# Kernel tuning notes

Measured on AMD Instinct MI355X. Metric: run time of the kernel, lower is better.

## Reference

```python
import jax, jax.numpy as jnp
import numpy as np

N, E = 50000, 300000
IN, FC, AC, H, C1, C2, OUT = 1024, 128, 20, 4, 10, 5, 3
FCN = FC + AC + H * C2  # 168


def bn_eval(x, g, b):
    # BatchNorm1d in eval mode with running_mean=0, running_var=1
    return x * (g / jnp.sqrt(1.0 + 1e-5)) + b


def add_self_loops(edge_index, edge_attr, n):
    # PyG add_self_loops with fill_value='mean': self-loop attr = mean of incoming edge attrs
    src, dst = edge_index[0], edge_index[1]
    ones = jnp.ones(src.shape[0], jnp.float32)
    deg = jax.ops.segment_sum(ones, dst, num_segments=n)
    mean_attr = jax.ops.segment_sum(edge_attr, dst, num_segments=n) / jnp.maximum(deg, 1.0)[:, None]
    loop = jnp.arange(n, dtype=src.dtype)
    return (jnp.concatenate([src, loop]), jnp.concatenate([dst, loop]),
            jnp.concatenate([edge_attr, mean_attr], 0))


def gatv2(x, src, dst, eattr, Wl, bl, Wr, br, We, att, b, n):
    # GATv2Conv (concat=True, negative_slope=0.2, edge_dim=1)
    h, c = att.shape
    xl = (x @ Wl + bl).reshape(n, h, c)
    xr = (x @ Wr + br).reshape(n, h, c)
    em = (eattr @ We).reshape(-1, h, c)
    m = jax.nn.leaky_relu(xl[src] + xr[dst] + em, 0.2)   # [E', H, C]
    logit = jnp.einsum('ehc,hc->eh', m, att)              # [E', H]
    mx = jax.ops.segment_max(logit, dst, num_segments=n)
    ex = jnp.exp(logit - mx[dst])
    den = jax.ops.segment_sum(ex, dst, num_segments=n)
    alpha = ex / (den[dst] + 1e-16)                       # segment softmax over dst
    out = jax.ops.segment_sum(xl[src] * alpha[..., None], dst, num_segments=n)
    return out.reshape(n, h * c) + b


def setup_inputs() -> dict:
    key = jax.random.key(0)
    ks = jax.random.split(key, 24)
    rn = lambda k, s: jax.random.normal(k, s, jnp.float32) * 0.05
    return {
        'features': jax.random.normal(ks[0], (N, IN), jnp.float32),
        'edges': jax.random.randint(ks[1], (2, E), 0, N),
        'edges2': jax.random.randint(ks[2], (2, E), 0, N),
        'edge_features': jax.random.normal(ks[3], (E, 1), jnp.float32),
        'additional_features': jax.random.normal(ks[4], (N, AC), jnp.float32),
        'sage_Wl': rn(ks[5], (IN, FC)), 'sage_bl': jnp.zeros((FC,), jnp.float32),
        'sage_Wr': rn(ks[6], (IN, FC)),
        'g1_Wl': rn(ks[7], (AC, H * C1)), 'g1_bl': jnp.zeros((H * C1,), jnp.float32),
        'g1_Wr': rn(ks[8], (AC, H * C1)), 'g1_br': jnp.zeros((H * C1,), jnp.float32),
        'g1_We': rn(ks[9], (1, H * C1)), 'g1_att': rn(ks[10], (H, C1)),
        'g1_b': jnp.zeros((H * C1,), jnp.float32),
        'g2_Wl': rn(ks[11], (H * C1, H * C2)), 'g2_bl': jnp.zeros((H * C2,), jnp.float32),
        'g2_Wr': rn(ks[12], (H * C1, H * C2)), 'g2_br': jnp.zeros((H * C2,), jnp.float32),
        'g2_We': rn(ks[13], (1, H * C2)), 'g2_att': rn(ks[14], (H, C2)),
        'g2_b': jnp.zeros((H * C2,), jnp.float32),
        'fc1_W': rn(ks[15], (FCN, FCN)), 'fc1_b': jnp.zeros((FCN,), jnp.float32),
        'fc2_W': rn(ks[16], (FCN, OUT)), 'fc2_b': jnp.zeros((OUT,), jnp.float32),
        'bnx_g': jnp.ones((FC,), jnp.float32), 'bnx_b': jnp.zeros((FC,), jnp.float32),
        'bny_g': jnp.ones((H * C2,), jnp.float32), 'bny_b': jnp.zeros((H * C2,), jnp.float32),
        'bnf_g': jnp.ones((FCN,), jnp.float32), 'bnf_b': jnp.zeros((FCN,), jnp.float32),
    }


def reference(features, edges, edges2, edge_features, additional_features,
              sage_Wl, sage_bl, sage_Wr,
              g1_Wl, g1_bl, g1_Wr, g1_br, g1_We, g1_att, g1_b,
              g2_Wl, g2_bl, g2_Wr, g2_br, g2_We, g2_att, g2_b,
              fc1_W, fc1_b, fc2_W, fc2_b,
              bnx_g, bnx_b, bny_g, bny_b, bnf_g, bnf_b):
    n = features.shape[0]
    # --- SAGEConv (mean aggr): out = lin_l(mean_j x_j) + lin_r(x_i) ---
    src, dst = edges[0], edges[1]
    deg = jax.ops.segment_sum(jnp.ones(src.shape[0], jnp.float32), dst, num_segments=n)
    aggr = jax.ops.segment_sum(features[src], dst, num_segments=n) / jnp.maximum(deg, 1.0)[:, None]
    x = aggr @ sage_Wl + sage_bl + features @ sage_Wr
    x = bn_eval(x, bnx_g, bnx_b)
    # --- GATv2 stack (self loops with mean edge-attr fill) ---
    s2, d2, ea = add_self_loops(edges2, edge_features, n)
    y = gatv2(additional_features, s2, d2, ea, g1_Wl, g1_bl, g1_Wr, g1_br, g1_We, g1_att, g1_b, n)
    y = jax.nn.leaky_relu(y, 0.01)  # activation (dropout off in eval)
    y = gatv2(y, s2, d2, ea, g2_Wl, g2_bl, g2_Wr, g2_br, g2_We, g2_att, g2_b, n)
    y = bn_eval(y, bny_g, bny_b)
    # --- MLP head ---
    z = jax.nn.leaky_relu(jnp.concatenate([x, y], axis=1), 0.01)
    z = jnp.concatenate([z, additional_features], axis=1) @ fc1_W + fc1_b
    z = jax.nn.relu(bn_eval(z, bnf_g, bnf_b))
    return z @ fc2_W + fc2_b
```

## Files before the change

### kernel.cpp

```cpp
#include <hip/hip_runtime.h>
#include <hip/hip_bf16.h>
#include <cfloat>

__device__ __forceinline__ float lrelu(float x, float a) { return x > 0.0f ? x : a * x; }

__device__ __forceinline__ unsigned short f2bf(float f) {
    unsigned u = __float_as_uint(f);
    unsigned r = (u + 0x7FFFu + ((u >> 16) & 1u)) >> 16;
    return (unsigned short)r;
}
__device__ __forceinline__ float bf2f(unsigned short u) {
    return __uint_as_float((unsigned)u << 16);
}

typedef __attribute__((ext_vector_type(8))) short short8;
typedef __attribute__((ext_vector_type(4))) float f32x4;

#define BN_RSQ 0.99999500003749968750f
#define SCAN_B 256

__global__ void zero_ws(uint4* __restrict__ p, int n16)
{
    int t = blockIdx.x * blockDim.x + threadIdx.x;
    if (t < n16) p[t] = make_uint4(0u, 0u, 0u, 0u);
// ... 45 lines not shown
        int j = idx & 7, lane = (idx >> 3) & 63, q = idx >> 9;
        int fn = q % 3, t = q / 3;
        int c = fn * 16 + (lane & 15);
        int k = t * 32 + (lane >> 4) * 8 + j;
        float v = 0.0f;
        if (k < 40 && c < 40) v = (c < 20) ? g2Wl[(size_t)k * 20 + c] : g2Wr[(size_t)k * 20 + (c - 20)];
        Bg2[idx] = f2bf(v);
        return;
    }
    idx -= 3072;
    if (idx < E) {
        atomicAdd(&cnt1[e1d[idx]], 1);
        int d2 = e2d[idx];
        atomicAdd(&cnt2[d2], 1);
        atomicAdd(&easum[d2], ef[idx]);
    }
}

__global__ __launch_bounds__(256) void gemm_sage_mfma(
    const float* __restrict__ A, const unsigned short* __restrict__ Btp,
    unsigned short* __restrict__ P, int M)
{
    __shared__ unsigned short As2[2][64][72];
    const int tid = threadIdx.x;
    const int wid = tid >> 6, lane = tid & 63;
    const int m0 = blockIdx.x * 64;
    const int l16 = lane & 15, g = lane >> 4;
    const int colbase = wid * 64 + l16;
    const short8* Bv = reinterpret_cast<const short8*>(Btp);
    const int srow = tid >> 4, scol = (tid & 15) * 4;

    f32x4 acc[4][4] = {};
    float4 rcur[4], rnext[4];

#pragma unroll
    for (int p = 0; p < 4; ++p) {
        int ar = m0 + p * 16 + srow;
        rcur[p] = make_float4(0.f, 0.f, 0.f, 0.f);
        if (ar < M) rcur[p] = *reinterpret_cast<const float4*>(&A[(size_t)ar * 1024 + scol]);
    }
#pragma unroll
    for (int p = 0; p < 4; ++p) {
        ushort4 u;
        u.x = f2bf(rcur[p].x); u.y = f2bf(rcur[p].y); u.z = f2bf(rcur[p].z); u.w = f2bf(rcur[p].w);
        *reinterpret_cast<ushort4*>(&As2[0][p * 16 + srow][scol]) = u;
    }
#pragma unroll
    for (int p = 0; p < 4; ++p) {
        int ar = m0 + p * 16 + srow;
        rcur[p] = make_float4(0.f, 0.f, 0.f, 0.f);
        if (ar < M) rcur[p] = *reinterpret_cast<const float4*>(&A[(size_t)ar * 1024 + 64 + scol]);
    }
    __syncthreads();

    for (int c = 0; c < 16; ++c) {
        const int buf = c & 1;
        if (c < 14) {
            const int k0 = (c + 2) * 64;
#pragma unroll
            for (int p = 0; p < 4; ++p) {
                int ar = m0 + p * 16 + srow;
                rnext[p] = make_float4(0.f, 0.f, 0.f, 0.f);
                if (ar < M) rnext[p] = *reinterpret_cast<const float4*>(&A[(size_t)ar * 1024 + k0 + scol]);
            }
        }
#pragma unroll
        for (int t = 0; t < 2; ++t) {
            const int ks = c * 2 + t;
            short8 afr[4], bfr[4];
#pragma unroll
            for (int fm = 0; fm < 4; ++fm)
                afr[fm] = *reinterpret_cast<const short8*>(&As2[buf][fm * 16 + l16][t * 32 + g * 8]);
#pragma unroll
            for (int fn = 0; fn < 4; ++fn)
                bfr[fn] = Bv[((ks * 4 + wid) * 4 + fn) * 64 + lane];
#pragma unroll
            for (int fm = 0; fm < 4; ++fm)
#pragma unroll
                for (int fn = 0; fn < 4; ++fn)
                    acc[fm][fn] = __builtin_amdgcn_mfma_f32_16x16x32_bf16(
                        afr[fm], bfr[fn], acc[fm][fn], 0, 0, 0);
        }
        if (c < 15) {
#pragma unroll
            for (int p = 0; p < 4; ++p) {
                ushort4 u;
                u.x = f2bf(rcur[p].x); u.y = f2bf(rcur[p].y);
                u.z = f2bf(rcur[p].z); u.w = f2bf(rcur[p].w);
                *reinterpret_cast<ushort4*>(&As2[buf ^ 1][p * 16 + srow][scol]) = u;
            }
        }
        __syncthreads();
#pragma unroll
        for (int p = 0; p < 4; ++p) rcur[p] = rnext[p];
    }

#pragma unroll
    for (int fm = 0; fm < 4; ++fm) {
#pragma unroll
        for (int r = 0; r < 4; ++r) {
            int row = m0 + fm * 16 + g * 4 + r;
            if (row < M) {
#pragma unroll
                for (int fn = 0; fn < 4; ++fn)
                    P[(size_t)row * 256 + colbase + fn * 16] = f2bf(acc[fm][fn][r]);
            }
        }
    }
}

template <int IND, int KS, int NF, int MODE>
__global__ __launch_bounds__(64) void gat_lin_mfma(
    const float* __restrict__ X, const unsigned short* __restrict__ Bp,
    const float* __restrict__ bl, const float* __restrict__ br,
    float* __restrict__ xl, float* __restrict__ xr, int M)
{
    constexpr int W = KS * 32;
    constexpr int WP = W + 8;
    __shared__ unsigned short xs[64][WP];
    const int lane = threadIdx.x;
    const int m0 = blockIdx.x * 64;
    const int l16 = lane & 15, g = lane >> 4;
    const short8* Bv = reinterpret_cast<const short8*>(Bp);

    constexpr int NV = 64 * IND / 4 / 64;
#pragma unroll
    for (int i = 0; i < NV; ++i) {
        int q = i * 64 + lane;
        int f = q * 4;
        int row = f / IND, col = f % IND;
        int ar = m0 + row;
        float4 v = make_float4(0.f, 0.f, 0.f, 0.f);
        if (ar < M) v = *reinterpret_cast<const float4*>(&X[(size_t)ar * IND + col]);
        ushort4 u;
        u.x = f2bf(v.x); u.y = f2bf(v.y); u.z = f2bf(v.z); u.w = f2bf(v.w);
        *reinterpret_cast<ushort4*>(&xs[row][col]) = u;
    }
    ushort4 zz; zz.x = 0; zz.y = 0; zz.z = 0; zz.w = 0;
#pragma unroll
    for (int c = IND; c < W; c += 4)
        *reinterpret_cast<ushort4*>(&xs[lane][c]) = zz;

    f32x4 acc[4][NF] = {};
#pragma unroll
    for (int t = 0; t < KS; ++t) {
        short8 afr[4], bfr[NF];
#pragma unroll
        for (int fm = 0; fm < 4; ++fm)
            afr[fm] = *reinterpret_cast<const short8*>(&xs[fm * 16 + l16][t * 32 + g * 8]);
#pragma unroll
        for (int fn = 0; fn < NF; ++fn)
            bfr[fn] = Bv[(t * NF + fn) * 64 + lane];
#pragma unroll
        for (int fm = 0; fm < 4; ++fm)
#pragma unroll
            for (int fn = 0; fn < NF; ++fn)
                acc[fm][fn] = __builtin_amdgcn_mfma_f32_16x16x32_bf16(
                    afr[fm], bfr[fn], acc[fm][fn], 0, 0, 0);
    }

#pragma unroll
    for (int fm = 0; fm < 4; ++fm) {
#pragma unroll
        for (int r = 0; r < 4; ++r) {
            int row = m0 + fm * 16 + g * 4 + r;
            if (row < M) {
#pragma unroll
                for (int fn = 0; fn < NF; ++fn) {
                    int col = fn * 16 + l16;
                    float v = acc[fm][fn][r];
                    if (MODE == 1) {
                        if (col < 40) {
                            int h = col / 10, c = col % 10;
                            xl[((size_t)row * 4 + h) * 12 + c] = v + bl[col];
                        } else if (col < 80) {
                            int cc = col - 40, h = cc / 10, c = cc % 10;
                            xr[((size_t)row * 4 + h) * 12 + c] = v + br[cc];
                        }
                    } else {
                        if (col < 20) {
                            int h = col / 5, c = col % 5;
                            xl[((size_t)row * 4 + h) * 8 + c] = v + bl[col];
                        } else if (col < 40) {
                            int cc = col - 20, h = cc / 5, c = cc % 5;
                            xr[((size_t)row * 4 + h) * 8 + c] = v + br[cc];
                        }
                    }
                }
            }
        }
    }
}

__global__ __launch_bounds__(256) void mlp_mfma(
    const unsigned short* __restrict__ z, const float* __restrict__ addf,
    const unsigned short* __restrict__ Bt1p,
    const float* __restrict__ fc1b, const float* __restrict__ bnfg, const float* __restrict__ bnfb,
    const float* __restrict__ fc2W, const float* __restrict__ fc2b,
    float* __restrict__ out, int M)
{
    __shared__ __align__(16) char smem[64 * 169 * 4];
    unsigned short (*zs)[200] = reinterpret_cast<unsigned short(*)[200]>(smem);
    float (*ts)[169] = reinterpret_cast<float(*)[169]>(smem);
    const int tid = threadIdx.x;
    const int wid = tid >> 6, lane = tid & 63;
    const int m0 = blockIdx.x * 64;
    const int l16 = lane & 15, g = lane >> 4;
    const short8* Bv = reinterpret_cast<const short8*>(Bt1p);

#pragma unroll
    for (int p = 0; p < 13; ++p) {
        int idx = p * 256 + tid;
        if (idx < 3200) {
            int row = idx / 50, c4 = (idx % 50) * 4;
            int ar = m0 + row;
            ushort4 u; u.x = 0; u.y = 0; u.z = 0; u.w = 0;
            if (ar < M) {
                if (c4 < 148) {
                    u = *reinterpret_cast<const ushort4*>(&z[(size_t)ar * 168 + c4]);
                } else if (c4 < 168) {
                    float4 v = *reinterpret_cast<const float4*>(&addf[(size_t)ar * 20 + (c4 - 148)]);
                    u.x = f2bf(v.x); u.y = f2bf(v.y); u.z = f2bf(v.z); u.w = f2bf(v.w);
                }
            }
            *reinterpret_cast<ushort4*>(&zs[row][c4]) = u;
        }
    }
    __syncthreads();

    f32x4 acc[4][4] = {};
    if (wid < 3) {
#pragma unroll
        for (int t = 0; t < 6; ++t) {
            short8 afr[4], bfr[4];
#pragma unroll
            for (int fm = 0; fm < 4; ++fm)
                afr[fm] = *reinterpret_cast<const short8*>(&zs[fm * 16 + l16][t * 32 + g * 8]);
#pragma unroll
            for (int fn = 0; fn < 4; ++fn)
                bfr[fn] = Bv[((t * 3 + wid) * 4 + fn) * 64 + lane];
#pragma unroll
            for (int fm = 0; fm < 4; ++fm)
#pragma unroll
                for (int fn = 0; fn < 4; ++fn)
                    acc[fm][fn] = __builtin_amdgcn_mfma_f32_16x16x32_bf16(
                        afr[fm], bfr[fn], acc[fm][fn], 0, 0, 0);
        }
    }
    __syncthreads();
    if (wid < 3) {
        const int colbase = wid * 64 + l16;
#pragma unroll
        for (int fm = 0; fm < 4; ++fm) {
#pragma unroll
            for (int r = 0; r < 4; ++r) {
                int rr = fm * 16 + g * 4 + r;
#pragma unroll
                for (int fn = 0; fn < 4; ++fn) {
                    int col = colbase + fn * 16;
                    if (col < 168) {
                        float v = acc[fm][fn][r] + fc1b[col];
                        v = v * (bnfg[col] * BN_RSQ) + bnfb[col];
                        ts[rr][col] = fmaxf(v, 0.0f);
                    }
                }
            }
        }
    }
    __syncthreads();
    if (tid < 192) {
        int r = tid & 63, c = tid >> 6;
        float acc2 = fc2b[c];
#pragma unroll 4
        for (int k = 0; k < 168; ++k) acc2 += ts[r][k] * fc2W[k * 3 + c];
        int row = m0 + r;
        if (row < M) out[(size_t)row * 3 + c] = acc2;
    }
}

__global__ void scan1(const int* __restrict__ cnt1, const int* __restrict__ cnt2,
                      int* __restrict__ off1, int* __restrict__ off2,
                      int* __restrict__ bsum1, int* __restrict__ bsum2, int M)
{
    __shared__ int sh[SCAN_B];
    int y = blockIdx.y;
    const int* cnt = y ? cnt2 : cnt1;
    int* excl = y ? off2 : off1;
    int* bsum = y ? bsum2 : bsum1;
    int i = blockIdx.x * SCAN_B + threadIdx.x;
    int v = (i < M) ? cnt[i] + y : 0;
    sh[threadIdx.x] = v;
// ... 30 lines not shown
                      const float* __restrict__ easum, float* __restrict__ ealoop, int M)
{
    int y = blockIdx.y;
    int* off = y ? off2 : off1;
    const int* bsum = y ? bsum2 : bsum1;
    const int* cnt = y ? cnt2 : cnt1;
    int i = blockIdx.x * SCAN_B + threadIdx.x;
    if (i < M) {
        int v = off[i] + bsum[blockIdx.x];
        off[i] = v;
        if (i == M - 1) off[M] = v + cnt[i] + y;
        if (y) ealoop[i] = easum[i] / fmaxf((float)cnt2[i], 1.0f);
    }
}

__global__ void fill_both(const int* __restrict__ e1s, const int* __restrict__ e1d,
                          const int* __restrict__ e2s, const int* __restrict__ e2d,
                          const float* __restrict__ ef, const float* __restrict__ ealoop,
                          const int* __restrict__ off1, const int* __restrict__ off2,
                          int* __restrict__ cnt1, int* __restrict__ cnt2,
                          int* __restrict__ srcs1, int2* __restrict__ se2, int E, int Eext)
{
    int t = blockIdx.x * blockDim.x + threadIdx.x;
    if (t < E) {
        int d = e1d[t];
        int pos = atomicSub(&cnt1[d], 1) - 1;
        srcs1[off1[d] + pos] = e1s[t];
    }
    int t2 = t - E;
    if (t2 >= 0 && t2 < Eext) {
        if (t2 < E) {
            int d = e2d[t2];
            int pos = atomicSub(&cnt2[d], 1) - 1;
            se2[off2[d] + pos] = make_int2(e2s[t2], __float_as_int(ef[t2]));
        } else {
            int nn = t2 - E;
            se2[off2[nn + 1] - 1] = make_int2(nn, __float_as_int(ealoop[nn]));
        }
    }
}

__global__ void sage_gather(const int* __restrict__ srcs1, const int* __restrict__ off1,
                            const unsigned short* __restrict__ P, const float* __restrict__ bl,
                            const float* __restrict__ bng, const float* __restrict__ bnb,
                            unsigned short* __restrict__ z, int N)
{
    int t = blockIdx.x * blockDim.x + threadIdx.x;
    if (t >= N * 16) return;
    int n = t >> 4, g = t & 15;
    int beg = off1[n], end = off1[n + 1];
    float a[8] = {};
    for (int j = beg; j < end; ++j) {
        int s = srcs1[j];
        short8 v = *reinterpret_cast<const short8*>(&P[(size_t)s * 256 + g * 8]);
#pragma unroll
        for (int k = 0; k < 8; ++k) a[k] += bf2f((unsigned short)v[k]);
    }
    float inv = 1.0f / fmaxf((float)(end - beg), 1.0f);
    short8 pr = *reinterpret_cast<const short8*>(&P[(size_t)n * 256 + 128 + g * 8]);
    short8 zo;
#pragma unroll
    for (int k = 0; k < 8; ++k) {
        int cc = g * 8 + k;
        float x = a[k] * inv + bl[cc] + bf2f((unsigned short)pr[k]);
        x = x * (bng[cc] * BN_RSQ) + bnb[cc];
        zo[k] = (short)f2bf(lrelu(x, 0.01f));
    }
    *reinterpret_cast<short8*>(&z[(size_t)n * 168 + g * 8]) = zo;
}

template <int H, int C, int PAD, int MODE>
__global__ void gat_node(const int2* __restrict__ se2, const int* __restrict__ off2,
                         const float* __restrict__ xl, const float* __restrict__ xr,
                         const float* __restrict__ We, const float* __restrict__ att,
                         const float* __restrict__ b,
                         const float* __restrict__ bng, const float* __restrict__ bnb,
                         void* __restrict__ outv, int N)
{
    int t = blockIdx.x * blockDim.x + threadIdx.x;
    if (t >= N * H) return;
    int n = t / H, h = t % H;

    float xrc[PAD], atth[PAD], weh[PAD];
    const float4* xrp = reinterpret_cast<const float4*>(&xr[((size_t)n * H + h) * PAD]);
#pragma unroll
    for (int q = 0; q < PAD / 4; ++q) {
        float4 v = xrp[q];
        xrc[q * 4 + 0] = v.x; xrc[q * 4 + 1] = v.y; xrc[q * 4 + 2] = v.z; xrc[q * 4 + 3] = v.w;
    }
#pragma unroll
    for (int c = 0; c < PAD; ++c) {
        atth[c] = (c < C) ? att[h * C + c] : 0.0f;
        weh[c]  = (c < C) ? We[h * C + c]  : 0.0f;
    }

    const int beg = off2[n], end = off2[n + 1];

    float mx = -FLT_MAX, den = 0.0f;
    float accv[PAD] = {};
    for (int j = beg; j < end; ++j) {
        int2 se = se2[j];
        int s = se.x;
        float ea = __int_as_float(se.y);
        const float4* xlp = reinterpret_cast<const float4*>(&xl[((size_t)s * H + h) * PAD]);
        float xv[PAD];
#pragma unroll
        for (int q = 0; q < PAD / 4; ++q) {
            float4 v = xlp[q];
            xv[q * 4 + 0] = v.x; xv[q * 4 + 1] = v.y; xv[q * 4 + 2] = v.z; xv[q * 4 + 3] = v.w;
        }
        float lg = 0.0f;
#pragma unroll
        for (int c = 0; c < PAD; ++c) {
            float m = xv[c] + xrc[c] + ea * weh[c];
            lg += lrelu(m, 0.2f) * atth[c];
        }
        if (lg > mx) {
            float sc = __expf(mx - lg);
            den *= sc;
#pragma unroll
            for (int c = 0; c < PAD; ++c) accv[c] *= sc;
            mx = lg;
        }
        float ex = __expf(lg - mx);
        den += ex;
#pragma unroll
        for (int c = 0; c < PAD; ++c) accv[c] += ex * xv[c];
    }
    float inv = 1.0f / (den + 1e-16f);

#pragma unroll
    for (int c = 0; c < C; ++c) {
        int jch = h * C + c;
        float v = accv[c] * inv + b[jch];
        if (MODE == 1) {
            ((float*)outv)[(size_t)n * (H * C) + jch] = lrelu(v, 0.01f);
        } else {
            v = v * (bng[jch] * BN_RSQ) + bnb[jch];
            ((unsigned short*)outv)[(size_t)n * 168 + 128 + jch] = f2bf(lrelu(v, 0.01f));
        }
    }
}

extern "C" void kernel_launch(void* const* d_in, const int* in_sizes, int n_in,
                              void* d_out, int out_size, void* d_ws, size_t ws_size,
                              hipStream_t stream)
{
    const float* features = (const float*)d_in[0];
    const int*   e1       = (const int*)d_in[1];
    const int*   e2       = (const int*)d_in[2];
    const float* ef       = (const float*)d_in[3];
    const float* addf     = (const float*)d_in[4];
    const float* sage_Wl  = (const float*)d_in[5];
    const float* sage_bl  = (const float*)d_in[6];
    const float* sage_Wr  = (const float*)d_in[7];
// ... 23 lines not shown
    const float* bnf_b = (const float*)d_in[31];

    const int N = in_sizes[0] / 1024;
    const int E = in_sizes[3];
    const int Eext = E + N;
    const int* e1s = e1, *e1d = e1 + E;
    const int* e2s = e2, *e2d = e2 + E;
    const int nb = (N + SCAN_B - 1) / SCAN_B;

    char* wb = (char*)d_ws;
    size_t off = 0;
    auto takeB = [&](size_t bytes) { char* p = wb + off; off = (off + bytes + 255) & ~(size_t)255; return p; };
    unsigned short* P = (unsigned short*)takeB((size_t)N * 256 * 2);
    unsigned short* z = (unsigned short*)takeB((size_t)N * 168 * 2);
    float* ealoop = (float*)takeB((size_t)N * 4);
    float* xl1   = (float*)takeB((size_t)N * 48 * 4);
    float* xr1   = (float*)takeB((size_t)N * 48 * 4);
    float* y1    = (float*)takeB((size_t)N * 40 * 4);
    float* xl2   = (float*)takeB((size_t)N * 32 * 4);
    float* xr2   = (float*)takeB((size_t)N * 32 * 4);
    unsigned short* Btp  = (unsigned short*)takeB((size_t)256 * 1024 * 2);
    unsigned short* Bt1p = (unsigned short*)takeB((size_t)36864 * 2);
    unsigned short* Bg1  = (unsigned short*)takeB((size_t)2560 * 2);
    unsigned short* Bg2  = (unsigned short*)takeB((size_t)3072 * 2);
    char* zero_beg = wb + off;
    int* cnt1    = (int*)takeB((size_t)N * 4);
    int* cnt2    = (int*)takeB((size_t)N * 4);
    float* easum = (float*)takeB((size_t)N * 4);
    size_t zero_len = (size_t)((wb + off) - zero_beg);
    int* off1  = (int*)takeB((size_t)(N + 1) * 4);
    int* off2  = (int*)takeB((size_t)(N + 1) * 4);
    int* bsum1 = (int*)takeB(SCAN_B * 4);
    int* bsum2 = (int*)takeB(SCAN_B * 4);
    int* srcs1 = (int*)takeB((size_t)E * 4);
    int2* se2  = (int2*)takeB((size_t)Eext * 8);
// ... 1 lines not shown
    const int B = 256;
    const int n16 = (int)(zero_len / 16);
    zero_ws<<<(n16 + B - 1) / B, B, 0, stream>>>((uint4*)zero_beg, n16);

    const int prep_total = 262144 + 36864 + 2560 + 3072 + E;
    prep_all<<<(prep_total + B - 1) / B, B, 0, stream>>>(
        sage_Wl, sage_Wr, Btp, fc1_W, Bt1p,
        g1_Wl, g1_Wr, Bg1, g2_Wl, g2_Wr, Bg2,
        e1d, e2d, ef, cnt1, cnt2, easum, E);

    scan1<<<dim3(nb, 2), SCAN_B, 0, stream>>>(cnt1, cnt2, off1, off2, bsum1, bsum2, N);
    scan2<<<dim3(1, 2), SCAN_B, 0, stream>>>(bsum1, bsum2, nb);
    scan3<<<dim3(nb, 2), SCAN_B, 0, stream>>>(off1, off2, bsum1, bsum2, cnt1, cnt2,
                                              easum, ealoop, N);

    fill_both<<<(E + Eext + B - 1) / B, B, 0, stream>>>(e1s, e1d, e2s, e2d, ef, ealoop,
                                                        off1, off2, cnt1, cnt2,
                                                        srcs1, se2, E, Eext);

    const int mtiles = (N + 63) / 64;
    gemm_sage_mfma<<<mtiles, 256, 0, stream>>>(features, Btp, P, N);
    sage_gather<<<(N * 16 + B - 1) / B, B, 0, stream>>>(srcs1, off1, P, sage_bl, bnx_g, bnx_b, z, N);

    gat_lin_mfma<20, 1, 5, 1><<<mtiles, 64, 0, stream>>>(addf, Bg1, g1_bl, g1_br, xl1, xr1, N);
    gat_node<4, 10, 12, 1><<<(N * 4 + B - 1) / B, B, 0, stream>>>(
        se2, off2, xl1, xr1, g1_We, g1_att, g1_b, nullptr, nullptr, (void*)y1, N);

    gat_lin_mfma<40, 2, 3, 2><<<mtiles, 64, 0, stream>>>(y1, Bg2, g2_bl, g2_br, xl2, xr2, N);
    gat_node<4, 5, 8, 2><<<(N * 4 + B - 1) / B, B, 0, stream>>>(
        se2, off2, xl2, xr2, g2_We, g2_att, g2_b, bny_g, bny_b, (void*)z, N);

    mlp_mfma<<<mtiles, 256, 0, stream>>>(z, addf, Bt1p, fc1_b, bnf_g, bnf_b, fc2_W, fc2_b,
                                         (float*)d_out, N);
}
```

Before: 296.8 us.

## Merge independent kernels into block-partitioned launches and store GAT projections as bf16

Independent stages (the SAGE GEMM, the CSR fill and the first GAT linear) are merged into one launch that routes each block by its index. The SAGE gather and the first GAT node aggregation share a second launch. This lets independent work overlap and cuts launch gaps. The GAT xl/xr intermediates are now stored in bf16 instead of fp32, which halves gather traffic at some cost in precision.

```diff
diff --git a/kernel.cpp b/kernel.cpp
--- a/kernel.cpp
+++ b/kernel.cpp
@@ -83,267 +83,6 @@
         int d2 = e2d[idx];
         atomicAdd(&cnt2[d2], 1);
         atomicAdd(&easum[d2], ef[idx]);
-    }
-}
-
-__global__ __launch_bounds__(256) void gemm_sage_mfma(
-    const float* __restrict__ A, const unsigned short* __restrict__ Btp,
-    unsigned short* __restrict__ P, int M)
-{
-    __shared__ unsigned short As2[2][64][72];
-    const int tid = threadIdx.x;
-    const int wid = tid >> 6, lane = tid & 63;
-    const int m0 = blockIdx.x * 64;
-    const int l16 = lane & 15, g = lane >> 4;
-    const int colbase = wid * 64 + l16;
-    const short8* Bv = reinterpret_cast<const short8*>(Btp);
-    const int srow = tid >> 4, scol = (tid & 15) * 4;
-
-    f32x4 acc[4][4] = {};
-    float4 rcur[4], rnext[4];
-
-#pragma unroll
-    for (int p = 0; p < 4; ++p) {
-        int ar = m0 + p * 16 + srow;
-        rcur[p] = make_float4(0.f, 0.f, 0.f, 0.f);
-        if (ar < M) rcur[p] = *reinterpret_cast<const float4*>(&A[(size_t)ar * 1024 + scol]);
-    }
-#pragma unroll
-    for (int p = 0; p < 4; ++p) {
-        ushort4 u;
-        u.x = f2bf(rcur[p].x); u.y = f2bf(rcur[p].y); u.z = f2bf(rcur[p].z); u.w = f2bf(rcur[p].w);
-        *reinterpret_cast<ushort4*>(&As2[0][p * 16 + srow][scol]) = u;
-    }
-#pragma unroll
-    for (int p = 0; p < 4; ++p) {
-        int ar = m0 + p * 16 + srow;
-        rcur[p] = make_float4(0.f, 0.f, 0.f, 0.f);
-        if (ar < M) rcur[p] = *reinterpret_cast<const float4*>(&A[(size_t)ar * 1024 + 64 + scol]);
-    }
-    __syncthreads();
-
-    for (int c = 0; c < 16; ++c) {
-        const int buf = c & 1;
-        if (c < 14) {
-            const int k0 = (c + 2) * 64;
-#pragma unroll
-            for (int p = 0; p < 4; ++p) {
-                int ar = m0 + p * 16 + srow;
-                rnext[p] = make_float4(0.f, 0.f, 0.f, 0.f);
-                if (ar < M) rnext[p] = *reinterpret_cast<const float4*>(&A[(size_t)ar * 1024 + k0 + scol]);
-            }
-        }
-#pragma unroll
-        for (int t = 0; t < 2; ++t) {
-            const int ks = c * 2 + t;
-            short8 afr[4], bfr[4];
-#pragma unroll
-            for (int fm = 0; fm < 4; ++fm)
-                afr[fm] = *reinterpret_cast<const short8*>(&As2[buf][fm * 16 + l16][t * 32 + g * 8]);
-#pragma unroll
-            for (int fn = 0; fn < 4; ++fn)
-                bfr[fn] = Bv[((ks * 4 + wid) * 4 + fn) * 64 + lane];
-#pragma unroll
-            for (int fm = 0; fm < 4; ++fm)
-#pragma unroll
-                for (int fn = 0; fn < 4; ++fn)
-                    acc[fm][fn] = __builtin_amdgcn_mfma_f32_16x16x32_bf16(
-                        afr[fm], bfr[fn], acc[fm][fn], 0, 0, 0);
-        }
-        if (c < 15) {
-#pragma unroll
-            for (int p = 0; p < 4; ++p) {
-                ushort4 u;
-                u.x = f2bf(rcur[p].x); u.y = f2bf(rcur[p].y);
-                u.z = f2bf(rcur[p].z); u.w = f2bf(rcur[p].w);
-                *reinterpret_cast<ushort4*>(&As2[buf ^ 1][p * 16 + srow][scol]) = u;
-            }
-        }
-        __syncthreads();
-#pragma unroll
-        for (int p = 0; p < 4; ++p) rcur[p] = rnext[p];
-    }
-
-#pragma unroll
-    for (int fm = 0; fm < 4; ++fm) {
-#pragma unroll
-        for (int r = 0; r < 4; ++r) {
-            int row = m0 + fm * 16 + g * 4 + r;
-            if (row < M) {
-#pragma unroll
-                for (int fn = 0; fn < 4; ++fn)
-                    P[(size_t)row * 256 + colbase + fn * 16] = f2bf(acc[fm][fn][r]);
-            }
-        }
-    }
-}
-
-template <int IND, int KS, int NF, int MODE>
-__global__ __launch_bounds__(64) void gat_lin_mfma(
-    const float* __restrict__ X, const unsigned short* __restrict__ Bp,
-    const float* __restrict__ bl, const float* __restrict__ br,
-    float* __restrict__ xl, float* __restrict__ xr, int M)
-{
-    constexpr int W = KS * 32;
-    constexpr int WP = W + 8;
-    __shared__ unsigned short xs[64][WP];
-    const int lane = threadIdx.x;
-    const int m0 = blockIdx.x * 64;
-    const int l16 = lane & 15, g = lane >> 4;
-    const short8* Bv = reinterpret_cast<const short8*>(Bp);
-
-    constexpr int NV = 64 * IND / 4 / 64;
-#pragma unroll
-    for (int i = 0; i < NV; ++i) {
-        int q = i * 64 + lane;
-        int f = q * 4;
-        int row = f / IND, col = f % IND;
-        int ar = m0 + row;
-        float4 v = make_float4(0.f, 0.f, 0.f, 0.f);
-        if (ar < M) v = *reinterpret_cast<const float4*>(&X[(size_t)ar * IND + col]);
-        ushort4 u;
-        u.x = f2bf(v.x); u.y = f2bf(v.y); u.z = f2bf(v.z); u.w = f2bf(v.w);
-        *reinterpret_cast<ushort4*>(&xs[row][col]) = u;
-    }
-    ushort4 zz; zz.x = 0; zz.y = 0; zz.z = 0; zz.w = 0;
-#pragma unroll
-    for (int c = IND; c < W; c += 4)
-        *reinterpret_cast<ushort4*>(&xs[lane][c]) = zz;
-
-    f32x4 acc[4][NF] = {};
-#pragma unroll
-    for (int t = 0; t < KS; ++t) {
-        short8 afr[4], bfr[NF];
-#pragma unroll
-        for (int fm = 0; fm < 4; ++fm)
-            afr[fm] = *reinterpret_cast<const short8*>(&xs[fm * 16 + l16][t * 32 + g * 8]);
-#pragma unroll
-        for (int fn = 0; fn < NF; ++fn)
-            bfr[fn] = Bv[(t * NF + fn) * 64 + lane];
-#pragma unroll
-        for (int fm = 0; fm < 4; ++fm)
-#pragma unroll
-            for (int fn = 0; fn < NF; ++fn)
-                acc[fm][fn] = __builtin_amdgcn_mfma_f32_16x16x32_bf16(
-                    afr[fm], bfr[fn], acc[fm][fn], 0, 0, 0);
-    }
-
-#pragma unroll
-    for (int fm = 0; fm < 4; ++fm) {
-#pragma unroll
-        for (int r = 0; r < 4; ++r) {
-            int row = m0 + fm * 16 + g * 4 + r;
-            if (row < M) {
-#pragma unroll
-                for (int fn = 0; fn < NF; ++fn) {
-                    int col = fn * 16 + l16;
-                    float v = acc[fm][fn][r];
-                    if (MODE == 1) {
-                        if (col < 40) {
-                            int h = col / 10, c = col % 10;
-                            xl[((size_t)row * 4 + h) * 12 + c] = v + bl[col];
-                        } else if (col < 80) {
-                            int cc = col - 40, h = cc / 10, c = cc % 10;
-                            xr[((size_t)row * 4 + h) * 12 + c] = v + br[cc];
-                        }
-                    } else {
-                        if (col < 20) {
-                            int h = col / 5, c = col % 5;
-                            xl[((size_t)row * 4 + h) * 8 + c] = v + bl[col];
-                        } else if (col < 40) {
-                            int cc = col - 20, h = cc / 5, c = cc % 5;
-                            xr[((size_t)row * 4 + h) * 8 + c] = v + br[cc];
-                        }
-                    }
-                }
-            }
-        }
-    }
-}
-
-__global__ __launch_bounds__(256) void mlp_mfma(
-    const unsigned short* __restrict__ z, const float* __restrict__ addf,
-    const unsigned short* __restrict__ Bt1p,
-    const float* __restrict__ fc1b, const float* __restrict__ bnfg, const float* __restrict__ bnfb,
-    const float* __restrict__ fc2W, const float* __restrict__ fc2b,
-    float* __restrict__ out, int M)
-{
-    __shared__ __align__(16) char smem[64 * 169 * 4];
-    unsigned short (*zs)[200] = reinterpret_cast<unsigned short(*)[200]>(smem);
-    float (*ts)[169] = reinterpret_cast<float(*)[169]>(smem);
-    const int tid = threadIdx.x;
-    const int wid = tid >> 6, lane = tid & 63;
-    const int m0 = blockIdx.x * 64;
-    const int l16 = lane & 15, g = lane >> 4;
-    const short8* Bv = reinterpret_cast<const short8*>(Bt1p);
-
-#pragma unroll
-    for (int p = 0; p < 13; ++p) {
-        int idx = p * 256 + tid;
-        if (idx < 3200) {
-            int row = idx / 50, c4 = (idx % 50) * 4;
-            int ar = m0 + row;
-            ushort4 u; u.x = 0; u.y = 0; u.z = 0; u.w = 0;
-            if (ar < M) {
-                if (c4 < 148) {
-                    u = *reinterpret_cast<const ushort4*>(&z[(size_t)ar * 168 + c4]);
-                } else if (c4 < 168) {
-                    float4 v = *reinterpret_cast<const float4*>(&addf[(size_t)ar * 20 + (c4 - 148)]);
-                    u.x = f2bf(v.x); u.y = f2bf(v.y); u.z = f2bf(v.z); u.w = f2bf(v.w);
-                }
-            }
-            *reinterpret_cast<ushort4*>(&zs[row][c4]) = u;
-        }
-    }
-    __syncthreads();
-
-    f32x4 acc[4][4] = {};
-    if (wid < 3) {
-#pragma unroll
-        for (int t = 0; t < 6; ++t) {
-            short8 afr[4], bfr[4];
-#pragma unroll
-            for (int fm = 0; fm < 4; ++fm)
-                afr[fm] = *reinterpret_cast<const short8*>(&zs[fm * 16 + l16][t * 32 + g * 8]);
-#pragma unroll
-            for (int fn = 0; fn < 4; ++fn)
-                bfr[fn] = Bv[((t * 3 + wid) * 4 + fn) * 64 + lane];
-#pragma unroll
-            for (int fm = 0; fm < 4; ++fm)
-#pragma unroll
-                for (int fn = 0; fn < 4; ++fn)
-                    acc[fm][fn] = __builtin_amdgcn_mfma_f32_16x16x32_bf16(
-                        afr[fm], bfr[fn], acc[fm][fn], 0, 0, 0);
-        }
-    }
-    __syncthreads();
-    if (wid < 3) {
-        const int colbase = wid * 64 + l16;
-#pragma unroll
-        for (int fm = 0; fm < 4; ++fm) {
-#pragma unroll
-            for (int r = 0; r < 4; ++r) {
-                int rr = fm * 16 + g * 4 + r;
-#pragma unroll
-                for (int fn = 0; fn < 4; ++fn) {
-                    int col = colbase + fn * 16;
-                    if (col < 168) {
-                        float v = acc[fm][fn][r] + fc1b[col];
-                        v = v * (bnfg[col] * BN_RSQ) + bnfb[col];
-                        ts[rr][col] = fmaxf(v, 0.0f);
-                    }
-                }
-            }
-        }
-    }
-    __syncthreads();
-    if (tid < 192) {
-        int r = tid & 63, c = tid >> 6;
-        float acc2 = fc2b[c];
-#pragma unroll 4
-        for (int k = 0; k < 168; ++k) acc2 += ts[r][k] * fc2W[k * 3 + c];
-        int row = m0 + r;
-        if (row < M) out[(size_t)row * 3 + c] = acc2;
     }
 }
 
@@ -404,104 +143,234 @@
     }
 }
 
-__global__ void fill_both(const int* __restrict__ e1s, const int* __restrict__ e1d,
-                          const int* __restrict__ e2s, const int* __restrict__ e2d,
-                          const float* __restrict__ ef, const float* __restrict__ ealoop,
-                          const int* __restrict__ off1, const int* __restrict__ off2,
-                          int* __restrict__ cnt1, int* __restrict__ cnt2,
-                          int* __restrict__ srcs1, int2* __restrict__ se2, int E, int Eext)
-{
-    int t = blockIdx.x * blockDim.x + threadIdx.x;
-    if (t < E) {
-        int d = e1d[t];
-        int pos = atomicSub(&cnt1[d], 1) - 1;
-        srcs1[off1[d] + pos] = e1s[t];
-    }
-    int t2 = t - E;
-    if (t2 >= 0 && t2 < Eext) {
-        if (t2 < E) {
-            int d = e2d[t2];
-            int pos = atomicSub(&cnt2[d], 1) - 1;
-            se2[off2[d] + pos] = make_int2(e2s[t2], __float_as_int(ef[t2]));
-        } else {
-            int nn = t2 - E;
-            se2[off2[nn + 1] - 1] = make_int2(nn, __float_as_int(ealoop[nn]));
-        }
-    }
-}
-
-__global__ void sage_gather(const int* __restrict__ srcs1, const int* __restrict__ off1,
-                            const unsigned short* __restrict__ P, const float* __restrict__ bl,
-                            const float* __restrict__ bng, const float* __restrict__ bnb,
-                            unsigned short* __restrict__ z, int N)
-{
-    int t = blockIdx.x * blockDim.x + threadIdx.x;
-    if (t >= N * 16) return;
-    int n = t >> 4, g = t & 15;
-    int beg = off1[n], end = off1[n + 1];
-    float a[8] = {};
-    for (int j = beg; j < end; ++j) {
-        int s = srcs1[j];
-        short8 v = *reinterpret_cast<const short8*>(&P[(size_t)s * 256 + g * 8]);
-#pragma unroll
-        for (int k = 0; k < 8; ++k) a[k] += bf2f((unsigned short)v[k]);
-    }
-    float inv = 1.0f / fmaxf((float)(end - beg), 1.0f);
-    short8 pr = *reinterpret_cast<const short8*>(&P[(size_t)n * 256 + 128 + g * 8]);
-    short8 zo;
-#pragma unroll
-    for (int k = 0; k < 8; ++k) {
-        int cc = g * 8 + k;
-        float x = a[k] * inv + bl[cc] + bf2f((unsigned short)pr[k]);
-        x = x * (bng[cc] * BN_RSQ) + bnb[cc];
-        zo[k] = (short)f2bf(lrelu(x, 0.01f));
-    }
-    *reinterpret_cast<short8*>(&z[(size_t)n * 168 + g * 8]) = zo;
-}
-
-template <int H, int C, int PAD, int MODE>
-__global__ void gat_node(const int2* __restrict__ se2, const int* __restrict__ off2,
-                         const float* __restrict__ xl, const float* __restrict__ xr,
-                         const float* __restrict__ We, const float* __restrict__ att,
-                         const float* __restrict__ b,
-                         const float* __restrict__ bng, const float* __restrict__ bnb,
-                         void* __restrict__ outv, int N)
-{
-    int t = blockIdx.x * blockDim.x + threadIdx.x;
-    if (t >= N * H) return;
-    int n = t / H, h = t % H;
-
-    float xrc[PAD], atth[PAD], weh[PAD];
-    const float4* xrp = reinterpret_cast<const float4*>(&xr[((size_t)n * H + h) * PAD]);
-#pragma unroll
-    for (int q = 0; q < PAD / 4; ++q) {
-        float4 v = xrp[q];
-        xrc[q * 4 + 0] = v.x; xrc[q * 4 + 1] = v.y; xrc[q * 4 + 2] = v.z; xrc[q * 4 + 3] = v.w;
-    }
-#pragma unroll
-    for (int c = 0; c < PAD; ++c) {
-        atth[c] = (c < C) ? att[h * C + c] : 0.0f;
-        weh[c]  = (c < C) ? We[h * C + c]  : 0.0f;
+__global__ __launch_bounds__(256) void stageA(
+    const float* __restrict__ A, const unsigned short* __restrict__ Btp,
+    unsigned short* __restrict__ P,
+    const int* __restrict__ e1s, const int* __restrict__ e1d,
+    const int* __restrict__ e2s, const int* __restrict__ e2d,
+    const float* __restrict__ ef, const float* __restrict__ ealoop,
+    const int* __restrict__ off1, const int* __restrict__ off2,
+    int* __restrict__ cnt1, int* __restrict__ cnt2,
+    int* __restrict__ srcs1, int2* __restrict__ se2,
+    const float* __restrict__ addf, const unsigned short* __restrict__ Bg1,
+    const float* __restrict__ g1bl, const float* __restrict__ g1br,
+    unsigned short* __restrict__ xl1b, unsigned short* __restrict__ xr1b,
+    int M, int E, int Eext, int Gg, int Gf)
+{
+    __shared__ __align__(16) char smem[20480];
+    const int bid = blockIdx.x;
+    const int tid = threadIdx.x;
+
+    if (bid < Gg) {
+        typedef unsigned short As2_t[64][72];
+        As2_t* As2 = reinterpret_cast<As2_t*>(smem);
+        const int wid = tid >> 6, lane = tid & 63;
+        const int m0 = bid * 64;
+        const int l16 = lane & 15, g = lane >> 4;
+        const int colbase = wid * 64 + l16;
+        const short8* Bv = reinterpret_cast<const short8*>(Btp);
+        const int srow = tid >> 4, scol = (tid & 15) * 4;
+
+        f32x4 acc[4][4] = {};
+        float4 rcur[4], rnext[4];
+
+#pragma unroll
+        for (int p = 0; p < 4; ++p) {
+            int ar = m0 + p * 16 + srow;
+            rcur[p] = make_float4(0.f, 0.f, 0.f, 0.f);
+            if (ar < M) rcur[p] = *reinterpret_cast<const float4*>(&A[(size_t)ar * 1024 + scol]);
+        }
+#pragma unroll
+        for (int p = 0; p < 4; ++p) {
+            ushort4 u;
+            u.x = f2bf(rcur[p].x); u.y = f2bf(rcur[p].y); u.z = f2bf(rcur[p].z); u.w = f2bf(rcur[p].w);
+            *reinterpret_cast<ushort4*>(&As2[0][p * 16 + srow][scol]) = u;
+        }
+#pragma unroll
+        for (int p = 0; p < 4; ++p) {
+            int ar = m0 + p * 16 + srow;
+            rcur[p] = make_float4(0.f, 0.f, 0.f, 0.f);
+            if (ar < M) rcur[p] = *reinterpret_cast<const float4*>(&A[(size_t)ar * 1024 + 64 + scol]);
+        }
+        __syncthreads();
+
+        for (int c = 0; c < 16; ++c) {
+            const int buf = c & 1;
+            if (c < 14) {
+                const int k0 = (c + 2) * 64;
+#pragma unroll
+                for (int p = 0; p < 4; ++p) {
+                    int ar = m0 + p * 16 + srow;
+                    rnext[p] = make_float4(0.f, 0.f, 0.f, 0.f);
+                    if (ar < M) rnext[p] = *reinterpret_cast<const float4*>(&A[(size_t)ar * 1024 + k0 + scol]);
+                }
+            }
+#pragma unroll
+            for (int t = 0; t < 2; ++t) {
+                const int ks = c * 2 + t;
+                short8 afr[4], bfr[4];
+#pragma unroll
+                for (int fm = 0; fm < 4; ++fm)
+                    afr[fm] = *reinterpret_cast<const short8*>(&As2[buf][fm * 16 + l16][t * 32 + g * 8]);
+#pragma unroll
+                for (int fn = 0; fn < 4; ++fn)
+                    bfr[fn] = Bv[((ks * 4 + wid) * 4 + fn) * 64 + lane];
+#pragma unroll
+                for (int fm = 0; fm < 4; ++fm)
+#pragma unroll
+                    for (int fn = 0; fn < 4; ++fn)
+                        acc[fm][fn] = __builtin_amdgcn_mfma_f32_16x16x32_bf16(
+                            afr[fm], bfr[fn], acc[fm][fn], 0, 0, 0);
+            }
+            if (c < 15) {
+#pragma unroll
+                for (int p = 0; p < 4; ++p) {
+                    ushort4 u;
+                    u.x = f2bf(rcur[p].x); u.y = f2bf(rcur[p].y);
+                    u.z = f2bf(rcur[p].z); u.w = f2bf(rcur[p].w);
+                    *reinterpret_cast<ushort4*>(&As2[buf ^ 1][p * 16 + srow][scol]) = u;
+                }
+            }
+            __syncthreads();
+#pragma unroll
+            for (int p = 0; p < 4; ++p) rcur[p] = rnext[p];
+        }
+
+#pragma unroll
+        for (int fm = 0; fm < 4; ++fm) {
+#pragma unroll
+            for (int r = 0; r < 4; ++r) {
+                int row = m0 + fm * 16 + g * 4 + r;
+                if (row < M) {
+#pragma unroll
+                    for (int fn = 0; fn < 4; ++fn)
+                        P[(size_t)row * 256 + colbase + fn * 16] = f2bf(acc[fm][fn][r]);
+                }
+            }
+        }
+    } else if (bid < Gg + Gf) {
+        int t = (bid - Gg) * 256 + tid;
+        if (t < E) {
+            int d = e1d[t];
+            int pos = atomicSub(&cnt1[d], 1) - 1;
+            srcs1[off1[d] + pos] = e1s[t];
+        }
+        int t2 = t - E;
+        if (t2 >= 0 && t2 < Eext) {
+            if (t2 < E) {
+                int d = e2d[t2];
+                int pos = atomicSub(&cnt2[d], 1) - 1;
+                se2[off2[d] + pos] = make_int2(e2s[t2], __float_as_int(ef[t2]));
+            } else {
+                int nn = t2 - E;
+                se2[off2[nn + 1] - 1] = make_int2(nn, __float_as_int(ealoop[nn]));
+            }
+        }
+    } else {
+        const int wid = tid >> 6, lane = tid & 63;
+        const int tile = (bid - Gg - Gf) * 4 + wid;
+        const int m0 = tile * 64;
+        if (m0 >= M) return;
+        unsigned short (*xs)[40] = reinterpret_cast<unsigned short(*)[40]>(smem + wid * 5120);
+        const int l16 = lane & 15, g = lane >> 4;
+        const short8* Bv = reinterpret_cast<const short8*>(Bg1);
+
+#pragma unroll
+        for (int i = 0; i < 5; ++i) {
+            int q = i * 64 + lane;
+            int f = q * 4;
+            int row = f / 20, col = f % 20;
+            int ar = m0 + row;
+            float4 v = make_float4(0.f, 0.f, 0.f, 0.f);
+            if (ar < M) v = *reinterpret_cast<const float4*>(&addf[(size_t)ar * 20 + col]);
+            ushort4 u;
+            u.x = f2bf(v.x); u.y = f2bf(v.y); u.z = f2bf(v.z); u.w = f2bf(v.w);
+            *reinterpret_cast<ushort4*>(&xs[row][col]) = u;
+        }
+        ushort4 zz; zz.x = 0; zz.y = 0; zz.z = 0; zz.w = 0;
+#pragma unroll
+        for (int c = 20; c < 32; c += 4)
+            *reinterpret_cast<ushort4*>(&xs[lane][c]) = zz;
+
+        f32x4 acc[4][5] = {};
+        short8 afr[4], bfr[5];
+#pragma unroll
+        for (int fm = 0; fm < 4; ++fm)
+            afr[fm] = *reinterpret_cast<const short8*>(&xs[fm * 16 + l16][g * 8]);
+#pragma unroll
+        for (int fn = 0; fn < 5; ++fn)
+            bfr[fn] = Bv[fn * 64 + lane];
+#pragma unroll
+        for (int fm = 0; fm < 4; ++fm)
+#pragma unroll
+            for (int fn = 0; fn < 5; ++fn)
+                acc[fm][fn] = __builtin_amdgcn_mfma_f32_16x16x32_bf16(
+                    afr[fm], bfr[fn], acc[fm][fn], 0, 0, 0);
+
+#pragma unroll
+        for (int fm = 0; fm < 4; ++fm) {
+#pragma unroll
+            for (int r = 0; r < 4; ++r) {
+                int row = m0 + fm * 16 + g * 4 + r;
+                if (row < M) {
+#pragma unroll
+                    for (int fn = 0; fn < 5; ++fn) {
+                        int col = fn * 16 + l16;
+                        float v = acc[fm][fn][r];
+                        if (col < 40) {
+                            int h = col / 10, c = col % 10;
+                            xl1b[((size_t)row * 4 + h) * 16 + c] = f2bf(v + g1bl[col]);
+                        } else if (col < 80) {
+                            int cc = col - 40, h = cc / 10, c = cc % 10;
+                            xr1b[((size_t)row * 4 + h) * 16 + c] = f2bf(v + g1br[cc]);
+                        }
+                    }
+                }
+            }
+        }
+    }
+}
+
+template <int H, int C, int BPAD, int MODE>
+__device__ __forceinline__ void gat_node_core(
+    const int2* __restrict__ se2, const int* __restrict__ off2,
+    const unsigned short* __restrict__ xlb, const unsigned short* __restrict__ xrb,
+    const float* __restrict__ We, const float* __restrict__ att,
+    const float* __restrict__ b,
+    const float* __restrict__ bng, const float* __restrict__ bnb,
+    void* __restrict__ outv, int n, int h)
+{
+    float xrc[C], atth[C], weh[C];
+    {
+        short8 sv[BPAD / 8];
+#pragma unroll
+        for (int q = 0; q < BPAD / 8; ++q)
+            sv[q] = *reinterpret_cast<const short8*>(&xrb[((size_t)n * H + h) * BPAD + q * 8]);
+#pragma unroll
+        for (int c = 0; c < C; ++c) xrc[c] = bf2f((unsigned short)sv[c / 8][c % 8]);
+    }
+#pragma unroll
+    for (int c = 0; c < C; ++c) {
+        atth[c] = att[h * C + c];
+        weh[c]  = We[h * C + c];
     }
 
     const int beg = off2[n], end = off2[n + 1];
-
     float mx = -FLT_MAX, den = 0.0f;
-    float accv[PAD] = {};
+    float accv[C] = {};
     for (int j = beg; j < end; ++j) {
         int2 se = se2[j];
         int s = se.x;
         float ea = __int_as_float(se.y);
-        const float4* xlp = reinterpret_cast<const float4*>(&xl[((size_t)s * H + h) * PAD]);
-        float xv[PAD];
-#pragma unroll
-        for (int q = 0; q < PAD / 4; ++q) {
-            float4 v = xlp[q];
-            xv[q * 4 + 0] = v.x; xv[q * 4 + 1] = v.y; xv[q * 4 + 2] = v.z; xv[q * 4 + 3] = v.w;
-        }
+        short8 sv[BPAD / 8];
+#pragma unroll
+        for (int q = 0; q < BPAD / 8; ++q)
+            sv[q] = *reinterpret_cast<const short8*>(&xlb[((size_t)s * H + h) * BPAD + q * 8]);
+        float xv[C];
         float lg = 0.0f;
 #pragma unroll
-        for (int c = 0; c < PAD; ++c) {
+        for (int c = 0; c < C; ++c) {
+            xv[c] = bf2f((unsigned short)sv[c / 8][c % 8]);
             float m = xv[c] + xrc[c] + ea * weh[c];
             lg += lrelu(m, 0.2f) * atth[c];
         }
@@ -509,13 +378,13 @@
             float sc = __expf(mx - lg);
             den *= sc;
 #pragma unroll
-            for (int c = 0; c < PAD; ++c) accv[c] *= sc;
+            for (int c = 0; c < C; ++c) accv[c] *= sc;
             mx = lg;
         }
         float ex = __expf(lg - mx);
         den += ex;
 #pragma unroll
-        for (int c = 0; c < PAD; ++c) accv[c] += ex * xv[c];
+        for (int c = 0; c < C; ++c) accv[c] += ex * xv[c];
     }
     float inv = 1.0f / (den + 1e-16f);
 
@@ -529,6 +398,215 @@
             v = v * (bng[jch] * BN_RSQ) + bnb[jch];
             ((unsigned short*)outv)[(size_t)n * 168 + 128 + jch] = f2bf(lrelu(v, 0.01f));
         }
+    }
+}
+
+__global__ void stageB(const int* __restrict__ srcs1, const int* __restrict__ off1,
+                       const unsigned short* __restrict__ P, const float* __restrict__ bl,
+                       const float* __restrict__ bng, const float* __restrict__ bnb,
+                       unsigned short* __restrict__ z,
+                       const int2* __restrict__ se2, const int* __restrict__ off2,
+                       const unsigned short* __restrict__ xl1b, const unsigned short* __restrict__ xr1b,
+                       const float* __restrict__ g1We, const float* __restrict__ g1att,
+                       const float* __restrict__ g1b, float* __restrict__ y1,
+                       int N, int Gg)
+{
+    const int bid = blockIdx.x;
+    if (bid < Gg) {
+        int t = bid * 256 + threadIdx.x;
+        if (t >= N * 16) return;
+        int n = t >> 4, g = t & 15;
+        int beg = off1[n], end = off1[n + 1];
+        float a[8] = {};
+        for (int j = beg; j < end; ++j) {
+            int s = srcs1[j];
+            short8 v = *reinterpret_cast<const short8*>(&P[(size_t)s * 256 + g * 8]);
+#pragma unroll
+            for (int k = 0; k < 8; ++k) a[k] += bf2f((unsigned short)v[k]);
+        }
+        float inv = 1.0f / fmaxf((float)(end - beg), 1.0f);
+        short8 pr = *reinterpret_cast<const short8*>(&P[(size_t)n * 256 + 128 + g * 8]);
+        short8 zo;
+#pragma unroll
+        for (int k = 0; k < 8; ++k) {
+            int cc = g * 8 + k;
+            float x = a[k] * inv + bl[cc] + bf2f((unsigned short)pr[k]);
+            x = x * (bng[cc] * BN_RSQ) + bnb[cc];
+            zo[k] = (short)f2bf(lrelu(x, 0.01f));
+        }
+        *reinterpret_cast<short8*>(&z[(size_t)n * 168 + g * 8]) = zo;
+    } else {
+        int t = (bid - Gg) * 256 + threadIdx.x;
+        if (t >= N * 4) return;
+        gat_node_core<4, 10, 16, 1>(se2, off2, xl1b, xr1b, g1We, g1att, g1b,
+                                    nullptr, nullptr, (void*)y1, t >> 2, t & 3);
+    }
+}
+
+__global__ __launch_bounds__(64) void gat_lin2_mfma(
+    const float* __restrict__ X, const unsigned short* __restrict__ Bp,
+    const float* __restrict__ bl, const float* __restrict__ br,
+    unsigned short* __restrict__ xlb, unsigned short* __restrict__ xrb, int M)
+{
+    __shared__ unsigned short xs[64][72];
+    const int lane = threadIdx.x;
+    const int m0 = blockIdx.x * 64;
+    const int l16 = lane & 15, g = lane >> 4;
+    const short8* Bv = reinterpret_cast<const short8*>(Bp);
+
+#pragma unroll
+    for (int i = 0; i < 10; ++i) {
+        int q = i * 64 + lane;
+        int f = q * 4;
+        int row = f / 40, col = f % 40;
+        int ar = m0 + row;
+        float4 v = make_float4(0.f, 0.f, 0.f, 0.f);
+        if (ar < M) v = *reinterpret_cast<const float4*>(&X[(size_t)ar * 40 + col]);
+        ushort4 u;
+        u.x = f2bf(v.x); u.y = f2bf(v.y); u.z = f2bf(v.z); u.w = f2bf(v.w);
+        *reinterpret_cast<ushort4*>(&xs[row][col]) = u;
+    }
+    ushort4 zz; zz.x = 0; zz.y = 0; zz.z = 0; zz.w = 0;
+#pragma unroll
+    for (int c = 40; c < 64; c += 4)
+        *reinterpret_cast<ushort4*>(&xs[lane][c]) = zz;
+
+    f32x4 acc[4][3] = {};
+#pragma unroll
+    for (int t = 0; t < 2; ++t) {
+        short8 afr[4], bfr[3];
+#pragma unroll
+        for (int fm = 0; fm < 4; ++fm)
+            afr[fm] = *reinterpret_cast<const short8*>(&xs[fm * 16 + l16][t * 32 + g * 8]);
+#pragma unroll
+        for (int fn = 0; fn < 3; ++fn)
+            bfr[fn] = Bv[(t * 3 + fn) * 64 + lane];
+#pragma unroll
+        for (int fm = 0; fm < 4; ++fm)
+#pragma unroll
+            for (int fn = 0; fn < 3; ++fn)
+                acc[fm][fn] = __builtin_amdgcn_mfma_f32_16x16x32_bf16(
+                    afr[fm], bfr[fn], acc[fm][fn], 0, 0, 0);
+    }
+
+#pragma unroll
+    for (int fm = 0; fm < 4; ++fm) {
+#pragma unroll
+        for (int r = 0; r < 4; ++r) {
+            int row = m0 + fm * 16 + g * 4 + r;
+            if (row < M) {
+#pragma unroll
+                for (int fn = 0; fn < 3; ++fn) {
+                    int col = fn * 16 + l16;
+                    float v = acc[fm][fn][r];
+                    if (col < 20) {
+                        int h = col / 5, c = col % 5;
+                        xlb[((size_t)row * 4 + h) * 8 + c] = f2bf(v + bl[col]);
+                    } else if (col < 40) {
+                        int cc = col - 20, h = cc / 5, c = cc % 5;
+                        xrb[((size_t)row * 4 + h) * 8 + c] = f2bf(v + br[cc]);
+                    }
+                }
+            }
+        }
+    }
+}
+
+__global__ void gat_node2(const int2* __restrict__ se2, const int* __restrict__ off2,
+                          const unsigned short* __restrict__ xlb, const unsigned short* __restrict__ xrb,
+                          const float* __restrict__ We, const float* __restrict__ att,
+                          const float* __restrict__ b,
+                          const float* __restrict__ bng, const float* __restrict__ bnb,
+                          unsigned short* __restrict__ z, int N)
+{
+    int t = blockIdx.x * blockDim.x + threadIdx.x;
+    if (t >= N * 4) return;
+    gat_node_core<4, 5, 8, 2>(se2, off2, xlb, xrb, We, att, b, bng, bnb, (void*)z, t >> 2, t & 3);
+}
+
+__global__ __launch_bounds__(256) void mlp_mfma(
+    const unsigned short* __restrict__ z, const float* __restrict__ addf,
+    const unsigned short* __restrict__ Bt1p,
+    const float* __restrict__ fc1b, const float* __restrict__ bnfg, const float* __restrict__ bnfb,
+    const float* __restrict__ fc2W, const float* __restrict__ fc2b,
+    float* __restrict__ out, int M)
+{
+    __shared__ __align__(16) char smem[64 * 169 * 4];
+    unsigned short (*zs)[200] = reinterpret_cast<unsigned short(*)[200]>(smem);
+    float (*ts)[169] = reinterpret_cast<float(*)[169]>(smem);
+    const int tid = threadIdx.x;
+    const int wid = tid >> 6, lane = tid & 63;
+    const int m0 = blockIdx.x * 64;
+    const int l16 = lane & 15, g = lane >> 4;
+    const short8* Bv = reinterpret_cast<const short8*>(Bt1p);
+
+#pragma unroll
+    for (int p = 0; p < 13; ++p) {
+        int idx = p * 256 + tid;
+        if (idx < 3200) {
+            int row = idx / 50, c4 = (idx % 50) * 4;
+            int ar = m0 + row;
+            ushort4 u; u.x = 0; u.y = 0; u.z = 0; u.w = 0;
+            if (ar < M) {
+                if (c4 < 148) {
+                    u = *reinterpret_cast<const ushort4*>(&z[(size_t)ar * 168 + c4]);
+                } else if (c4 < 168) {
+                    float4 v = *reinterpret_cast<const float4*>(&addf[(size_t)ar * 20 + (c4 - 148)]);
+                    u.x = f2bf(v.x); u.y = f2bf(v.y); u.z = f2bf(v.z); u.w = f2bf(v.w);
+                }
+            }
+            *reinterpret_cast<ushort4*>(&zs[row][c4]) = u;
+        }
+    }
+    __syncthreads();
+
+    f32x4 acc[4][4] = {};
+    if (wid < 3) {
+#pragma unroll
+        for (int t = 0; t < 6; ++t) {
+            short8 afr[4], bfr[4];
+#pragma unroll
+            for (int fm = 0; fm < 4; ++fm)
+                afr[fm] = *reinterpret_cast<const short8*>(&zs[fm * 16 + l16][t * 32 + g * 8]);
+#pragma unroll
+            for (int fn = 0; fn < 4; ++fn)
+                bfr[fn] = Bv[((t * 3 + wid) * 4 + fn) * 64 + lane];
+#pragma unroll
+            for (int fm = 0; fm < 4; ++fm)
+#pragma unroll
+                for (int fn = 0; fn < 4; ++fn)
+                    acc[fm][fn] = __builtin_amdgcn_mfma_f32_16x16x32_bf16(
+                        afr[fm], bfr[fn], acc[fm][fn], 0, 0, 0);
+        }
+    }
+    __syncthreads();
+    if (wid < 3) {
+        const int colbase = wid * 64 + l16;
+#pragma unroll
+        for (int fm = 0; fm < 4; ++fm) {
+#pragma unroll
+            for (int r = 0; r < 4; ++r) {
+                int rr = fm * 16 + g * 4 + r;
+#pragma unroll
+                for (int fn = 0; fn < 4; ++fn) {
+                    int col = colbase + fn * 16;
+                    if (col < 168) {
+                        float v = acc[fm][fn][r] + fc1b[col];
+                        v = v * (bnfg[col] * BN_RSQ) + bnfb[col];
+                        ts[rr][col] = fmaxf(v, 0.0f);
+                    }
+                }
+            }
+        }
+    }
+    __syncthreads();
+    if (tid < 192) {
+        int r = tid & 63, c = tid >> 6;
+        float acc2 = fc2b[c];
+#pragma unroll 4
+        for (int k = 0; k < 168; ++k) acc2 += ts[r][k] * fc2W[k * 3 + c];
+        int row = m0 + r;
+        if (row < M) out[(size_t)row * 3 + c] = acc2;
     }
 }
 
@@ -582,11 +660,11 @@
     unsigned short* P = (unsigned short*)takeB((size_t)N * 256 * 2);
     unsigned short* z = (unsigned short*)takeB((size_t)N * 168 * 2);
     float* ealoop = (float*)takeB((size_t)N * 4);
-    float* xl1   = (float*)takeB((size_t)N * 48 * 4);
-    float* xr1   = (float*)takeB((size_t)N * 48 * 4);
-    float* y1    = (float*)takeB((size_t)N * 40 * 4);
-    float* xl2   = (float*)takeB((size_t)N * 32 * 4);
-    float* xr2   = (float*)takeB((size_t)N * 32 * 4);
+    unsigned short* xl1b = (unsigned short*)takeB((size_t)N * 64 * 2);
+    unsigned short* xr1b = (unsigned short*)takeB((size_t)N * 64 * 2);
+    float* y1 = (float*)takeB((size_t)N * 40 * 4);
+    unsigned short* xl2b = (unsigned short*)takeB((size_t)N * 32 * 2);
+    unsigned short* xr2b = (unsigned short*)takeB((size_t)N * 32 * 2);
     unsigned short* Btp  = (unsigned short*)takeB((size_t)256 * 1024 * 2);
     unsigned short* Bt1p = (unsigned short*)takeB((size_t)36864 * 2);
     unsigned short* Bg1  = (unsigned short*)takeB((size_t)2560 * 2);
@@ -618,21 +696,24 @@
     scan3<<<dim3(nb, 2), SCAN_B, 0, stream>>>(off1, off2, bsum1, bsum2, cnt1, cnt2,
                                               easum, ealoop, N);
 
-    fill_both<<<(E + Eext + B - 1) / B, B, 0, stream>>>(e1s, e1d, e2s, e2d, ef, ealoop,
-                                                        off1, off2, cnt1, cnt2,
-                                                        srcs1, se2, E, Eext);
-
     const int mtiles = (N + 63) / 64;
-    gemm_sage_mfma<<<mtiles, 256, 0, stream>>>(features, Btp, P, N);
-    sage_gather<<<(N * 16 + B - 1) / B, B, 0, stream>>>(srcs1, off1, P, sage_bl, bnx_g, bnx_b, z, N);
-
-    gat_lin_mfma<20, 1, 5, 1><<<mtiles, 64, 0, stream>>>(addf, Bg1, g1_bl, g1_br, xl1, xr1, N);
-    gat_node<4, 10, 12, 1><<<(N * 4 + B - 1) / B, B, 0, stream>>>(
-        se2, off2, xl1, xr1, g1_We, g1_att, g1_b, nullptr, nullptr, (void*)y1, N);
-
-    gat_lin_mfma<40, 2, 3, 2><<<mtiles, 64, 0, stream>>>(y1, Bg2, g2_bl, g2_br, xl2, xr2, N);
-    gat_node<4, 5, 8, 2><<<(N * 4 + B - 1) / B, B, 0, stream>>>(
-        se2, off2, xl2, xr2, g2_We, g2_att, g2_b, bny_g, bny_b, (void*)z, N);
+    const int Gf = (E + Eext + B - 1) / B;
+    const int Gl = (mtiles + 3) / 4;
+    stageA<<<mtiles + Gf + Gl, 256, 0, stream>>>(
+        features, Btp, P,
+        e1s, e1d, e2s, e2d, ef, ealoop, off1, off2, cnt1, cnt2, srcs1, se2,
+        addf, Bg1, g1_bl, g1_br, xl1b, xr1b,
+        N, E, Eext, mtiles, Gf);
+
+    const int Gg = (N * 16 + B - 1) / B;
+    const int Gn = (N * 4 + B - 1) / B;
+    stageB<<<Gg + Gn, 256, 0, stream>>>(
+        srcs1, off1, P, sage_bl, bnx_g, bnx_b, z,
+        se2, off2, xl1b, xr1b, g1_We, g1_att, g1_b, y1, N, Gg);
+
+    gat_lin2_mfma<<<mtiles, 64, 0, stream>>>(y1, Bg2, g2_bl, g2_br, xl2b, xr2b, N);
+    gat_node2<<<Gn, 256, 0, stream>>>(se2, off2, xl2b, xr2b, g2_We, g2_att, g2_b,
+                                      bny_g, bny_b, z, N);
 
     mlp_mfma<<<mtiles, 256, 0, stream>>>(z, addf, Bt1p, fc1_b, bnf_g, bnf_b, fc2_W, fc2_b,
                                          (float*)d_out, N);
```

New measurement: 260.6 us. 1.14x faster.
